# Performance work log

Measured on AMD Instinct MI355X. Metric: run time of the kernel, lower is better.

## Reference

```python
import jax, jax.numpy as jnp
import numpy as np

N = 50000     # nodes
E = 800000    # edges
D = 64        # hidesize (= out_channels per head)
H = 5         # heads
C = 64        # per-head channels (concat=False -> mean over heads, C == D)
NEG_SLOPE = 0.2
LN_EPS = 1e-5


def setup_inputs() -> dict:
    key = jax.random.key(0)
    ks = jax.random.split(key, 16)
    s = 0.05
    return {
        "features": jax.random.normal(ks[0], (N, D), dtype=jnp.float32),
        "edge_index": jax.random.randint(ks[1], (2, E), 0, N, dtype=jnp.int64),
        "rel_emb_vector": jax.random.normal(ks[2], (E, D), dtype=jnp.float32),
        # GATv2Conv params
        "Wl": jax.random.normal(ks[3], (D, H * C), dtype=jnp.float32) * s,
        "bl": jnp.zeros((H * C,), jnp.float32),
        "Wr": jax.random.normal(ks[4], (D, H * C), dtype=jnp.float32) * s,
        "br": jnp.zeros((H * C,), jnp.float32),
        "We": jax.random.normal(ks[5], (D, H * C), dtype=jnp.float32) * s,  # lin_edge, no bias
        "att": jax.random.normal(ks[6], (H, C), dtype=jnp.float32) * s,
        "conv_bias": jnp.zeros((C,), jnp.float32),
        # LayerNorms
        "ln_g": jnp.ones((D,), jnp.float32), "ln_b": jnp.zeros((D,), jnp.float32),
        "ln1_g": jnp.ones((D,), jnp.float32), "ln1_b": jnp.zeros((D,), jnp.float32),
        # MLP (activation resolved to None by the source bug)
        "fc_w": jax.random.normal(ks[7], (D, 2 * D), dtype=jnp.float32) * s,
        "fc_b": jnp.zeros((2 * D,), jnp.float32),
        "fc1_w": jax.random.normal(ks[8], (2 * D, D), dtype=jnp.float32) * s,
        "fc1_b": jnp.zeros((D,), jnp.float32),
    }


def _layernorm(x, g, b):
    m = x.mean(-1, keepdims=True)
    v = ((x - m) ** 2).mean(-1, keepdims=True)
    return (x - m) * jax.lax.rsqrt(v + LN_EPS) * g + b


def _gatv2_conv(x, edge_index, edge_attr, Wl, bl, Wr, br, We, att, conv_bias):
    src, dst = edge_index[0], edge_index[1]
    n = x.shape[0]
    # add_self_loops with fill_value='mean': self-loop edge_attr = mean of incoming edge_attr
    cnt = jax.ops.segment_sum(jnp.ones((edge_attr.shape[0],), x.dtype), dst, num_segments=n)
    loop_attr = jax.ops.segment_sum(edge_attr, dst, num_segments=n) / jnp.maximum(cnt, 1.0)[:, None]
    ar = jnp.arange(n, dtype=src.dtype)
    src2 = jnp.concatenate([src, ar])
    dst2 = jnp.concatenate([dst, ar])
    ea = jnp.concatenate([edge_attr, loop_attr], axis=0)        # [E+N, D]
    xl = (x @ Wl + bl).reshape(n, H, C)                          # source transform
    xr = (x @ Wr + br).reshape(n, H, C)                          # target transform
    em = (ea @ We).reshape(-1, H, C)
    m = jax.nn.leaky_relu(xl[src2] + xr[dst2] + em, NEG_SLOPE)   # [E+N, H, C]
    logits = jnp.einsum('ehc,hc->eh', m, att)                    # [E+N, H]
    # scatter-softmax over destination nodes (self loops guarantee nonempty segments)
    mx = jax.lax.stop_gradient(jax.ops.segment_max(logits, dst2, num_segments=n))
    z = jnp.exp(logits - mx[dst2])
    den = jax.ops.segment_sum(z, dst2, num_segments=n)
    alpha = z / den[dst2]                                        # [E+N, H]
    out = jax.ops.segment_sum(xl[src2] * alpha[:, :, None], dst2, num_segments=n)  # [N, H, C]
    return out.mean(axis=1) + conv_bias                          # concat=False -> head mean


def reference(features, edge_index, rel_emb_vector, Wl, bl, Wr, br, We, att, conv_bias,
              ln_g, ln_b, ln1_g, ln1_b, fc_w, fc_b, fc1_w, fc1_b):
    conv = _gatv2_conv(features, edge_index, rel_emb_vector, Wl, bl, Wr, br, We, att, conv_bias)
    x = _layernorm(features + conv, ln_g, ln_b)
    h = (x @ fc_w + fc_b) @ fc1_w + fc1_b   # activation=None, dropout in eval mode
    return _layernorm(x + h, ln1_g, ln1_b)
```

## Files before the change

kernel.cpp:

```cpp
#include <hip/hip_runtime.h>
#include <hip/hip_bf16.h>
#include <math.h>

#define LN_EPS 1e-5f
#define NEGS 0.2f

typedef short s8v __attribute__((ext_vector_type(8)));
typedef short s4v __attribute__((ext_vector_type(4)));
typedef float f4v __attribute__((ext_vector_type(4)));
typedef unsigned short ushort;

__device__ __forceinline__ float wredsum(float v) {
#pragma unroll
    for (int s = 32; s > 0; s >>= 1) v += __shfl_xor(v, s);
    return v;
}
__device__ __forceinline__ ushort f2bf(float x) {
    union { __hip_bfloat16 h; ushort u; } c;
    c.h = __float2bfloat16(x);
    return c.u;
}
__device__ __forceinline__ float bf2f(ushort u) {
    return __uint_as_float(((unsigned int)u) << 16);
}

__global__ void k_hist(const int* __restrict__ dst, int* __restrict__ cnt, int E) {
    int idx = blockIdx.x * blockDim.x + threadIdx.x;
    int stride = gridDim.x * blockDim.x;
    for (; idx < E; idx += stride) atomicAdd(&cnt[dst[idx]], 1);
}

__global__ __launch_bounds__(1024) void k_scanA(const int* __restrict__ cnt,
                                                int* __restrict__ bsum, int N) {
    __shared__ int ws[16];
    int tt = threadIdx.x, ln = tt & 63, wv = tt >> 6;
    int i = blockIdx.x * 1024 + tt;
    int v = (i < N) ? (cnt[i] + 1) : 0;
#pragma unroll
    for (int s = 32; s > 0; s >>= 1) v += __shfl_xor(v, s);
    if (ln == 0) ws[wv] = v;
    __syncthreads();
    if (tt == 0) {
        int s = 0;
#pragma unroll
        for (int k = 0; k < 16; k++) s += ws[k];
        bsum[blockIdx.x] = s;
    }
}
__global__ __launch_bounds__(64) void k_scanB(const int* __restrict__ bsum,
                                              int* __restrict__ bpre,
                                              int* __restrict__ roffN, int nb) {
    int ln = threadIdx.x;
    int v = (ln < nb) ? bsum[ln] : 0;
    int x = v;
#pragma unroll
    for (int off = 1; off < 64; off <<= 1) {
        int y = __shfl_up(x, off);
        if (ln >= off) x += y;
    }
    if (ln < nb) bpre[ln] = x - v;
    if (ln == 63) *roffN = x;
}
__global__ __launch_bounds__(1024) void k_scanC(const int* __restrict__ cnt,
                                                const int* __restrict__ bpre,
                                                int* __restrict__ roff,
                                                int* __restrict__ wpos, int N) {
    __shared__ int ws[16];
    int tt = threadIdx.x, ln = tt & 63, wv = tt >> 6;
    int i = blockIdx.x * 1024 + tt;
    int v = (i < N) ? (cnt[i] + 1) : 0;
    int x = v;
#pragma unroll
    for (int off = 1; off < 64; off <<= 1) {
        int y = __shfl_up(x, off);
        if (ln >= off) x += y;
    }
    if (ln == 63) ws[wv] = x;
    __syncthreads();
    if (wv == 0) {
        int wsv = (ln < 16) ? ws[ln] : 0;
        int xs = wsv;
#pragma unroll
        for (int off = 1; off < 16; off <<= 1) {
            int y = __shfl_up(xs, off);
            if (ln >= off) xs += y;
        }
        if (ln < 16) ws[ln] = xs - wsv;
    }
    __syncthreads();
    int excl = x - v + ws[wv] + bpre[blockIdx.x];
    if (i < N) { roff[i] = excl; wpos[i] = excl; }
}

__global__ void k_scatter(const int* __restrict__ src, const int* __restrict__ dst,
                          int* __restrict__ wpos, int* __restrict__ eidC,
                          int* __restrict__ srcC, int* __restrict__ posC, int E) {
    int idx = blockIdx.x * blockDim.x + threadIdx.x;
    int stride = gridDim.x * blockDim.x;
    for (; idx < E; idx += stride) {
        int d = dst[idx];
        int p = atomicAdd(&wpos[d], 1);
        eidC[p] = idx;
        srcC[p] = src[idx];
        posC[idx] = p;
    }
}

__global__ __launch_bounds__(256) void k_loopcsr(const int* __restrict__ eidC,
                                                 const int* __restrict__ roff,
                                                 const float* __restrict__ rel,
                                                 float* __restrict__ loopat,
                                                 int* __restrict__ srcC, int N) {
    int t = threadIdx.x, ln = t & 63, wv = t >> 6;
    int nw = gridDim.x * 4;
    for (int n = blockIdx.x * 4 + wv; n < N; n += nw) {
        int r0 = roff[n], r1 = roff[n + 1];
        int deg = r1 - r0 - 1;
        float s0 = 0.f, s1 = 0.f, s2 = 0.f, s3 = 0.f;
        int j = 0;
        for (; j + 4 <= deg; j += 4) {
            int e0 = eidC[r0 + j], e1 = eidC[r0 + j + 1];
            int e2 = eidC[r0 + j + 2], e3 = eidC[r0 + j + 3];
            s0 += rel[(long long)e0 * 64 + ln];
            s1 += rel[(long long)e1 * 64 + ln];
            s2 += rel[(long long)e2 * 64 + ln];
            s3 += rel[(long long)e3 * 64 + ln];
        }
        for (; j < deg; j++) s0 += rel[(long long)eidC[r0 + j] * 64 + ln];
        float s = (s0 + s1) + (s2 + s3);
        loopat[(long long)n * 64 + ln] = s / (float)(deg > 0 ? deg : 1);
        if (ln == 0) srcC[r1 - 1] = n;
    }
}

__global__ __launch_bounds__(512) void k_linC(const float* __restrict__ feat,
                                              const float* __restrict__ Wlg,
                                              const float* __restrict__ blg,
                                              const float* __restrict__ Wrg,
                                              const float* __restrict__ brg,
                                              ushort* __restrict__ xlbf,
                                              ushort* __restrict__ xrbf, int N) {
    __shared__ __align__(16) ushort wT[2][64 * 320];
    int t = threadIdx.x;
    for (int i = t; i < 5120; i += 512) {
        int mat = i >= 2560;
        int j = mat ? (i - 2560) : i;
        int n = j >> 3, kb = j & 7;
        const float* W = mat ? Wrg : Wlg;
        s8v v;
#pragma unroll
        for (int k = 0; k < 8; k++) v[k] = (short)f2bf(W[(kb * 8 + k) * 320 + n]);
        int by = (n * 128 + kb * 16) ^ ((n & 7) << 4);
        *(s8v*)((char*)&wT[mat][0] + by) = v;
    }
    __syncthreads();

    int l = t & 63, wv = t >> 6;
    int g = l >> 4, m = l & 15;
    int wstride = gridDim.x * 128;
    for (int r0 = (blockIdx.x * 8 + wv) * 16; r0 < N; r0 += wstride) {
        s8v afr[2];
        {
            long long row = (r0 + m < N) ? (r0 + m) : (N - 1);
#pragma unroll
            for (int kh = 0; kh < 2; kh++) {
                const float* p = feat + row * 64 + kh * 32 + g * 8;
                float4 u0 = *(const float4*)(p);
                float4 u1 = *(const float4*)(p + 4);
                s8v a;
                a[0] = (short)f2bf(u0.x); a[1] = (short)f2bf(u0.y);
                a[2] = (short)f2bf(u0.z); a[3] = (short)f2bf(u0.w);
                a[4] = (short)f2bf(u1.x); a[5] = (short)f2bf(u1.y);
                a[6] = (short)f2bf(u1.z); a[7] = (short)f2bf(u1.w);
                afr[kh] = a;
            }
        }
#pragma unroll
        for (int mat = 0; mat < 2; mat++) {
            const float* bias = mat ? brg : blg;
            ushort* y = mat ? xrbf : xlbf;
            const char* wb = (const char*)&wT[mat][0];
#pragma unroll
            for (int h = 0; h < 5; h++) {
                f4v acc[4];
#pragma unroll
                for (int ct = 0; ct < 4; ct++) acc[ct] = (f4v)0.0f;
#pragma unroll
                for (int ct = 0; ct < 4; ct++) {
                    int n = h * 64 + ct * 16 + m;
                    int b0 = (n * 128 + 0 * 64 + g * 16) ^ ((n & 7) << 4);
                    int b1 = (n * 128 + 1 * 64 + g * 16) ^ ((n & 7) << 4);
                    s8v bf0 = *(const s8v*)(wb + b0);
                    s8v bf1 = *(const s8v*)(wb + b1);
                    acc[ct] = __builtin_amdgcn_mfma_f32_16x16x32_bf16(afr[0], bf0, acc[ct], 0, 0, 0);
                    acc[ct] = __builtin_amdgcn_mfma_f32_16x16x32_bf16(afr[1], bf1, acc[ct], 0, 0, 0);
                }
                float bv[4];
#pragma unroll
                for (int ct = 0; ct < 4; ct++) bv[ct] = bias[h * 64 + ct * 16 + m];
#pragma unroll
                for (int q = 0; q < 4; q++) {
                    int row = r0 + g * 4 + q;
                    if (row < N) {
                        s4v o;
#pragma unroll
                        for (int ct = 0; ct < 4; ct++) o[ct] = (short)f2bf(acc[ct][q] + bv[ct]);
                        *(s4v*)(y + (long long)row * 320 + h * 64 + m * 4) = o;
                    }
                }
            }
        }
    }
}

__global__ __launch_bounds__(512) void k_fused(
    const float* __restrict__ rel, const float* __restrict__ loopat,
    const int* __restrict__ src, const int* __restrict__ dst,
    const ushort* __restrict__ xlbf, const ushort* __restrict__ xrbf,
    const float* __restrict__ Weg, const float* __restrict__ attg,
    const int* __restrict__ posC, const int* __restrict__ roff,
    float* __restrict__ logitsC, int E, int M) {
    __shared__ __align__(16) ushort weT[64 * 320];
    int t = threadIdx.x;
    for (int i = t; i < 2560; i += 512) {
        int n = i >> 3, kb = i & 7;
        s8v v;
#pragma unroll
        for (int k = 0; k < 8; k++) v[k] = (short)f2bf(Weg[(kb * 8 + k) * 320 + n]);
        int by = (n * 128 + kb * 16) ^ ((n & 7) << 4);
        *(s8v*)((char*)weT + by) = v;
    }
    __syncthreads();

    int l = t & 63, wv = t >> 6;
    int g = l >> 4, m = l & 15;
    int r0 = (blockIdx.x * 8 + wv) * 16;
    if (r0 >= M) return;

    s8v afr[2];
    {
        int row = r0 + m;
        if (row >= M) row = M - 1;
        const float* ap = (row < E) ? (rel + (long long)row * 64)
                                    : (loopat + (long long)(row - E) * 64);
#pragma unroll
        for (int kh = 0; kh < 2; kh++) {
            const float* p = ap + kh * 32 + g * 8;
            float4 u0 = *(const float4*)(p);
            float4 u1 = *(const float4*)(p + 4);
            s8v a;
            a[0] = (short)f2bf(u0.x); a[1] = (short)f2bf(u0.y);
            a[2] = (short)f2bf(u0.z); a[3] = (short)f2bf(u0.w);
            a[4] = (short)f2bf(u1.x); a[5] = (short)f2bf(u1.y);
            a[6] = (short)f2bf(u1.z); a[7] = (short)f2bf(u1.w);
            afr[kh] = a;
        }
    }

    const ushort* xptr[4];
    const ushort* rptr[4];
    int parr[4];
    bool vld[4];
#pragma unroll
    for (int q = 0; q < 4; q++) {
        int row = r0 + g * 4 + q;
        vld[q] = row < M;
        int rr = vld[q] ? row : (M - 1);
        int s, d, p;
        if (rr < E) { s = src[rr]; d = dst[rr]; p = posC[rr]; }
        else        { s = d = rr - E; p = roff[rr - E + 1] - 1; }
        xptr[q] = xlbf + (long long)s * 320 + m * 4;
        rptr[q] = xrbf + (long long)d * 320 + m * 4;
        parr[q] = p;
    }

    s4v xb[2][4], rb[2][4];
    float attb[2][4];
#pragma unroll
    for (int q = 0; q < 4; q++) {
        xb[0][q] = *(const s4v*)(xptr[q]);
        rb[0][q] = *(const s4v*)(rptr[q]);
    }
#pragma unroll
    for (int ct = 0; ct < 4; ct++) attb[0][ct] = attg[ct * 16 + m];

#pragma unroll
    for (int h = 0; h < 5; h++) {
        if (h < 4) {
#pragma unroll
            for (int q = 0; q < 4; q++) {
                xb[(h + 1) & 1][q] = *(const s4v*)(xptr[q] + (h + 1) * 64);
                rb[(h + 1) & 1][q] = *(const s4v*)(rptr[q] + (h + 1) * 64);
            }
#pragma unroll
            for (int ct = 0; ct < 4; ct++)
                attb[(h + 1) & 1][ct] = attg[(h + 1) * 64 + ct * 16 + m];
        }

        f4v acc[4];
#pragma unroll
        for (int ct = 0; ct < 4; ct++) acc[ct] = (f4v)0.0f;
#pragma unroll
        for (int ct = 0; ct < 4; ct++) {
            int n = h * 64 + ct * 16 + m;
            int b0 = (n * 128 + 0 * 64 + g * 16) ^ ((n & 7) << 4);
            int b1 = (n * 128 + 1 * 64 + g * 16) ^ ((n & 7) << 4);
            s8v bf0 = *(const s8v*)((const char*)weT + b0);
            s8v bf1 = *(const s8v*)((const char*)weT + b1);
            acc[ct] = __builtin_amdgcn_mfma_f32_16x16x32_bf16(afr[0], bf0, acc[ct], 0, 0, 0);
            acc[ct] = __builtin_amdgcn_mfma_f32_16x16x32_bf16(afr[1], bf1, acc[ct], 0, 0, 0);
        }

#pragma unroll
        for (int q = 0; q < 4; q++) {
            float sum = 0.f;
#pragma unroll
            for (int ct = 0; ct < 4; ct++) {
                float v = acc[ct][q] + bf2f((ushort)xb[h & 1][q][ct])
                                     + bf2f((ushort)rb[h & 1][q][ct]);
                v = v > 0.f ? v : v * NEGS;
                sum = fmaf(v, attb[h & 1][ct], sum);
            }
            sum += __shfl_xor(sum, 1);
            sum += __shfl_xor(sum, 2);
            sum += __shfl_xor(sum, 4);
            sum += __shfl_xor(sum, 8);
            if (vld[q] && m == 0) logitsC[(long long)parr[q] * 5 + h] = sum;
        }
    }
}

__global__ __launch_bounds__(256) void k_agg(const float* __restrict__ logitsC,
                                             const int* __restrict__ srcC,
                                             const int* __restrict__ roff,
                                             const ushort* __restrict__ xlbf,
                                             float* __restrict__ conv, int N) {
    int t = threadIdx.x, ln = t & 63, wv = t >> 6;
    int sub = ln >> 4, m = ln & 15;
    int nw = gridDim.x * 4;
    for (int n = blockIdx.x * 4 + wv; n < N; n += nw) {
        int r0 = roff[n], r1 = roff[n + 1];
        int deg = r1 - r0;
        float se[5] = {0.f, 0.f, 0.f, 0.f, 0.f};
        for (int j = ln; j < deg; j += 64) {
            long long base = (long long)(r0 + j) * 5;
#pragma unroll
            for (int h = 0; h < 5; h++) se[h] += expf(logitsC[base + h]);
        }
        float dh[5];
#pragma unroll
        for (int h = 0; h < 5; h++) dh[h] = 1.0f / wredsum(se[h]);
        float accv[4] = {0.f, 0.f, 0.f, 0.f};
        for (int jj = sub; jj < deg; jj += 4) {
            int slot = r0 + jj;
            int s = srcC[slot];
            const ushort* xp = xlbf + (long long)s * 320 + m * 4;
            long long lb = (long long)slot * 5;
#pragma unroll
            for (int h = 0; h < 5; h++) {
                float a = expf(logitsC[lb + h]) * dh[h];
                s4v xv = *(const s4v*)(xp + h * 64);
#pragma unroll
                for (int j = 0; j < 4; j++) accv[j] = fmaf(a, bf2f((ushort)xv[j]), accv[j]);
            }
        }
#pragma unroll
        for (int j = 0; j < 4; j++) {
            accv[j] += __shfl_xor(accv[j], 16);
            accv[j] += __shfl_xor(accv[j], 32);
        }
        float v0 = __shfl(accv[0], m);
        float v1 = __shfl(accv[1], m);
        float v2 = __shfl(accv[2], m);
        float v3 = __shfl(accv[3], m);
        float outv = (sub == 0) ? v0 : (sub == 1) ? v1 : (sub == 2) ? v2 : v3;
        conv[(long long)n * 64 + ln] = outv * 0.2f;
    }
}

__global__ __launch_bounds__(512) void k_mlp(const float* __restrict__ feat,
                                             const float* __restrict__ conv,
                                             const float* __restrict__ cbias,
                                             const float* __restrict__ lng,
                                             const float* __restrict__ lnb,
                                             const float* __restrict__ ln1g,
                                             const float* __restrict__ ln1b,
                                             const float* __restrict__ fcwg,
                                             const float* __restrict__ fcb,
                                             const float* __restrict__ fc1wg,
                                             const float* __restrict__ fc1b,
                                             float* __restrict__ out, int N) {
    __shared__ __align__(16) ushort w1T[64 * 128];
    __shared__ __align__(16) ushort w2T[64 * 128];
    __shared__ __align__(16) ushort tls[8][16 * 128];
    __shared__ __align__(16) ushort xnl[8][16 * 64];
    int t = threadIdx.x;
    for (int i = t; i < 8192; i += 512) {
        int k = i >> 7, n = i & 127;
        int by = (n * 128 + k * 2) ^ ((n & 7) << 4);
        w1T[by >> 1] = f2bf(fcwg[i]);
    }
    for (int i = t; i < 8192; i += 512) {
        int k = i >> 6, n = i & 63;
        int by = (n * 256 + k * 2) ^ ((n & 7) << 4);
        w2T[by >> 1] = f2bf(fc1wg[i]);
    }
    __syncthreads();
    int ln = t & 63, wv = t >> 6;
    int g = ln >> 4, m = ln & 15;
    char* tb = (char*)&tls[wv][0];
    char* xb = (char*)&xnl[wv][0];
    float fcbv[8];
#pragma unroll
    for (int ct = 0; ct < 8; ct++) fcbv[ct] = fcb[ct * 16 + m];
    float fc1bv[4], g1v[4], b1v[4];
#pragma unroll
    for (int ct = 0; ct < 4; ct++) {
        fc1bv[ct] = fc1b[ct * 16 + m];
        g1v[ct] = ln1g[ct * 16 + m];
        b1v[ct] = ln1b[ct * 16 + m];
    }
    int nblk = gridDim.x * 8;
    for (int nb0 = (blockIdx.x * 8 + wv) * 16; nb0 < N; nb0 += nblk * 16) {
        int node = nb0 + m;
        long long nd = (node < N) ? node : (N - 1);
        float xv[2][8];
#pragma unroll
        for (int kh = 0; kh < 2; kh++) {
            int c0 = kh * 32 + g * 8;
            const float* fp = feat + nd * 64 + c0;
            const float* cp = conv + nd * 64 + c0;
            float4 f0 = *(const float4*)fp, f1 = *(const float4*)(fp + 4);
            float4 q0 = *(const float4*)cp, q1 = *(const float4*)(cp + 4);
            float4 cb0 = *(const float4*)(cbias + c0), cb1 = *(const float4*)(cbias + c0 + 4);
            xv[kh][0] = f0.x + q0.x + cb0.x; xv[kh][1] = f0.y + q0.y + cb0.y;
            xv[kh][2] = f0.z + q0.z + cb0.z; xv[kh][3] = f0.w + q0.w + cb0.w;
            xv[kh][4] = f1.x + q1.x + cb1.x; xv[kh][5] = f1.y + q1.y + cb1.y;
            xv[kh][6] = f1.z + q1.z + cb1.z; xv[kh][7] = f1.w + q1.w + cb1.w;
        }
        float sm = 0.f;
#pragma unroll
        for (int kh = 0; kh < 2; kh++)
#pragma unroll
            for (int j = 0; j < 8; j++) sm += xv[kh][j];
        sm += __shfl_xor(sm, 16); sm += __shfl_xor(sm, 32);
        float mu = sm * (1.0f / 64.0f);
        float vr = 0.f;
#pragma unroll
        for (int kh = 0; kh < 2; kh++)
#pragma unroll
            for (int j = 0; j < 8; j++) {
                float dv = xv[kh][j] - mu;
                vr += dv * dv;
            }
        vr += __shfl_xor(vr, 16); vr += __shfl_xor(vr, 32);
        float rs = rsqrtf(vr * (1.0f / 64.0f) + LN_EPS);
        s8v af[2];
#pragma unroll
        for (int kh = 0; kh < 2; kh++) {
            int c0 = kh * 32 + g * 8;
            float4 g0 = *(const float4*)(lng + c0), g1 = *(const float4*)(lng + c0 + 4);
            float4 e0 = *(const float4*)(lnb + c0), e1 = *(const float4*)(lnb + c0 + 4);
            float gg[8] = {g0.x, g0.y, g0.z, g0.w, g1.x, g1.y, g1.z, g1.w};
            float bb[8] = {e0.x, e0.y, e0.z, e0.w, e1.x, e1.y, e1.z, e1.w};
#pragma unroll
            for (int j = 0; j < 8; j++)
                af[kh][j] = (short)f2bf((xv[kh][j] - mu) * rs * gg[j] + bb[j]);
            int by = (m * 128 + (kh * 32 + g * 8) * 2) ^ ((m & 7) << 4);
            *(s8v*)(xb + by) = af[kh];
        }
        f4v a1[8];
#pragma unroll
        for (int ct = 0; ct < 8; ct++) a1[ct] = (f4v)0.0f;
#pragma unroll
        for (int ct = 0; ct < 8; ct++) {
            int n1 = ct * 16 + m;
#pragma unroll
            for (int kh = 0; kh < 2; kh++) {
                int by = (n1 * 128 + (kh * 32 + g * 8) * 2) ^ ((n1 & 7) << 4);
                s8v bf = *(const s8v*)((const char*)w1T + by);
                a1[ct] = __builtin_amdgcn_mfma_f32_16x16x32_bf16(af[kh], bf, a1[ct], 0, 0, 0);
            }
        }
#pragma unroll
        for (int ct = 0; ct < 8; ct++)
#pragma unroll
            for (int q = 0; q < 4; q++) {
                int r = g * 4 + q, c = ct * 16 + m;
                int by = (r * 256 + c * 2) ^ ((r & 7) << 4);
                *(ushort*)(tb + by) = f2bf(a1[ct][q] + fcbv[ct]);
            }
        f4v a2[4];
#pragma unroll
        for (int ct = 0; ct < 4; ct++) a2[ct] = (f4v)0.0f;
#pragma unroll
        for (int kh2 = 0; kh2 < 4; kh2++) {
            int by = (m * 256 + (kh2 * 32 + g * 8) * 2) ^ ((m & 7) << 4);
            s8v a2f = *(const s8v*)(tb + by);
#pragma unroll
            for (int ct = 0; ct < 4; ct++) {
                int n2 = ct * 16 + m;
                int by2 = (n2 * 256 + (kh2 * 32 + g * 8) * 2) ^ ((n2 & 7) << 4);
                s8v bf = *(const s8v*)((const char*)w2T + by2);
                a2[ct] = __builtin_amdgcn_mfma_f32_16x16x32_bf16(a2f, bf, a2[ct], 0, 0, 0);
            }
        }
#pragma unroll
        for (int q = 0; q < 4; q++) {
            int r = g * 4 + q;
            float yv[4];
#pragma unroll
            for (int ct = 0; ct < 4; ct++) {
                int by = (r * 128 + (ct * 16 + m) * 2) ^ ((r & 7) << 4);
                yv[ct] = bf2f(*(const ushort*)(xb + by)) + a2[ct][q] + fc1bv[ct];
            }
            float sm2 = (yv[0] + yv[1]) + (yv[2] + yv[3]);
            sm2 += __shfl_xor(sm2, 1); sm2 += __shfl_xor(sm2, 2);
            sm2 += __shfl_xor(sm2, 4); sm2 += __shfl_xor(sm2, 8);
            float mu2 = sm2 * (1.0f / 64.0f);
            float vr2 = 0.f;
#pragma unroll
            for (int ct = 0; ct < 4; ct++) {
                float dv = yv[ct] - mu2;
                vr2 += dv * dv;
            }
            vr2 += __shfl_xor(vr2, 1); vr2 += __shfl_xor(vr2, 2);
            vr2 += __shfl_xor(vr2, 4); vr2 += __shfl_xor(vr2, 8);
            float rs2 = rsqrtf(vr2 * (1.0f / 64.0f) + LN_EPS);
            int rn = nb0 + r;
            if (rn < N) {
#pragma unroll
                for (int ct = 0; ct < 4; ct++)
                    out[(long long)rn * 64 + ct * 16 + m] =
                        (yv[ct] - mu2) * rs2 * g1v[ct] + b1v[ct];
            }
        }
    }
}

extern "C" void kernel_launch(void* const* d_in, const int* in_sizes, int n_in,
                              void* d_out, int out_size, void* d_ws, size_t ws_size,
                              hipStream_t stream) {
    const float* feat = (const float*)d_in[0];
    const int* ei = (const int*)d_in[1];
    const float* rel = (const float*)d_in[2];
    const float* Wl = (const float*)d_in[3];
    const float* bl = (const float*)d_in[4];
    const float* Wr = (const float*)d_in[5];
    const float* br = (const float*)d_in[6];
    const float* We = (const float*)d_in[7];
    const float* att = (const float*)d_in[8];
    const float* cbias = (const float*)d_in[9];
    const float* lng = (const float*)d_in[10];
    const float* lnb = (const float*)d_in[11];
    const float* ln1g = (const float*)d_in[12];
    const float* ln1b = (const float*)d_in[13];
    const float* fcw = (const float*)d_in[14];
    const float* fcb = (const float*)d_in[15];
    const float* fc1w = (const float*)d_in[16];
    const float* fc1b = (const float*)d_in[17];
    float* out = (float*)d_out;

    int N = in_sizes[0] / 64;
    int E = in_sizes[1] / 2;
    int M = E + N;
    const int* src = ei;
    const int* dst = ei + E;
    int nb = (N + 1023) / 1024;

    char* wsb = (char*)d_ws;
    ushort* xlbf = (ushort*)wsb;            wsb += (size_t)N * 320 * 2;
    ushort* xrbf = (ushort*)wsb;            wsb += (size_t)N * 320 * 2;
    float* loopat = (float*)wsb;            wsb += (size_t)N * 64 * 4;
    float* conv = (float*)wsb;              wsb += (size_t)N * 64 * 4;
    float* logitsC = (float*)wsb;           wsb += (size_t)M * 5 * 4;
    int* cnt = (int*)wsb;                   wsb += (size_t)N * 4;
    int* roff = (int*)wsb;                  wsb += (size_t)(N + 1) * 4;
    int* wpos = (int*)wsb;                  wsb += (size_t)N * 4;
    int* eidC = (int*)wsb;                  wsb += (size_t)M * 4;
    int* srcC = (int*)wsb;                  wsb += (size_t)M * 4;
    int* posC = (int*)wsb;                  wsb += (size_t)E * 4;
    int* bsum = (int*)wsb;                  wsb += 64 * 4;
    int* bpre = (int*)wsb;                  wsb += 64 * 4;

    hipMemsetAsync(cnt, 0, (size_t)N * 4, stream);

    k_hist<<<1024, 256, 0, stream>>>(dst, cnt, E);
    k_scanA<<<nb, 1024, 0, stream>>>(cnt, bsum, N);
    k_scanB<<<1, 64, 0, stream>>>(bsum, bpre, &roff[N], nb);
    k_scanC<<<nb, 1024, 0, stream>>>(cnt, bpre, roff, wpos, N);
    k_scatter<<<1024, 256, 0, stream>>>(src, dst, wpos, eidC, srcC, posC, E);
    k_loopcsr<<<2048, 256, 0, stream>>>(eidC, roff, rel, loopat, srcC, N);
    k_linC<<<(N + 127) / 128, 512, 0, stream>>>(feat, Wl, bl, Wr, br, xlbf, xrbf, N);
    k_fused<<<(M + 127) / 128, 512, 0, stream>>>(rel, loopat, src, dst, xlbf, xrbf, We, att,
                                                 posC, roff, logitsC, E, M);
    k_agg<<<2048, 256, 0, stream>>>(logitsC, srcC, roff, xlbf, conv, N);
    k_mlp<<<391, 512, 0, stream>>>(feat, conv, cbias, lng, lnb, ln1g, ln1b, fcw, fcb, fc1w, fc1b,
                                   out, N);
}
```

Baseline: 598.6 us.

## Iterate fused edge kernel in CSR order and use bit-trick bf16 conversion

The fused edge-logit kernel now walks edges in destination-sorted CSR slot order. It reads eidC/srcC/dstC arrays and writes logits contiguously instead of scattering through posC. The scatter kernel stores dstC rather than posC, and the self-loop slot fills eidC/srcC/dstC. This makes the xr gathers and logit writes more local, at the cost of an indirect gather of rel rows through eidC. The float-to-bf16 conversion is also replaced with an inline round-to-nearest-even bit manipulation, which does not handle NaN specially.

```diff
diff --git a/kernel.cpp b/kernel.cpp
--- a/kernel.cpp
+++ b/kernel.cpp
@@ -16,9 +16,9 @@
     return v;
 }
 __device__ __forceinline__ ushort f2bf(float x) {
-    union { __hip_bfloat16 h; ushort u; } c;
-    c.h = __float2bfloat16(x);
-    return c.u;
+    unsigned int u = __float_as_uint(x);
+    u += 0x7fffu + ((u >> 16) & 1u);
+    return (ushort)(u >> 16);
 }
 __device__ __forceinline__ float bf2f(ushort u) {
     return __uint_as_float(((unsigned int)u) << 16);
@@ -94,7 +94,7 @@
 
 __global__ void k_scatter(const int* __restrict__ src, const int* __restrict__ dst,
                           int* __restrict__ wpos, int* __restrict__ eidC,
-                          int* __restrict__ srcC, int* __restrict__ posC, int E) {
+                          int* __restrict__ srcC, int* __restrict__ dstC, int E) {
     int idx = blockIdx.x * blockDim.x + threadIdx.x;
     int stride = gridDim.x * blockDim.x;
     for (; idx < E; idx += stride) {
@@ -102,15 +102,17 @@
         int p = atomicAdd(&wpos[d], 1);
         eidC[p] = idx;
         srcC[p] = src[idx];
-        posC[idx] = p;
-    }
-}
-
-__global__ __launch_bounds__(256) void k_loopcsr(const int* __restrict__ eidC,
+        dstC[p] = d;
+    }
+}
+
+__global__ __launch_bounds__(256) void k_loopcsr(const int* __restrict__ eidC_ro,
                                                  const int* __restrict__ roff,
                                                  const float* __restrict__ rel,
                                                  float* __restrict__ loopat,
-                                                 int* __restrict__ srcC, int N) {
+                                                 int* __restrict__ eidC,
+                                                 int* __restrict__ srcC,
+                                                 int* __restrict__ dstC, int N, int E) {
     int t = threadIdx.x, ln = t & 63, wv = t >> 6;
     int nw = gridDim.x * 4;
     for (int n = blockIdx.x * 4 + wv; n < N; n += nw) {
@@ -119,17 +121,21 @@
         float s0 = 0.f, s1 = 0.f, s2 = 0.f, s3 = 0.f;
         int j = 0;
         for (; j + 4 <= deg; j += 4) {
-            int e0 = eidC[r0 + j], e1 = eidC[r0 + j + 1];
-            int e2 = eidC[r0 + j + 2], e3 = eidC[r0 + j + 3];
+            int e0 = eidC_ro[r0 + j], e1 = eidC_ro[r0 + j + 1];
+            int e2 = eidC_ro[r0 + j + 2], e3 = eidC_ro[r0 + j + 3];
             s0 += rel[(long long)e0 * 64 + ln];
             s1 += rel[(long long)e1 * 64 + ln];
             s2 += rel[(long long)e2 * 64 + ln];
             s3 += rel[(long long)e3 * 64 + ln];
         }
-        for (; j < deg; j++) s0 += rel[(long long)eidC[r0 + j] * 64 + ln];
+        for (; j < deg; j++) s0 += rel[(long long)eidC_ro[r0 + j] * 64 + ln];
         float s = (s0 + s1) + (s2 + s3);
         loopat[(long long)n * 64 + ln] = s / (float)(deg > 0 ? deg : 1);
-        if (ln == 0) srcC[r1 - 1] = n;
+        if (ln == 0) {
+            eidC[r1 - 1] = E + n;
+            srcC[r1 - 1] = n;
+            dstC[r1 - 1] = n;
+        }
     }
 }
 
@@ -215,10 +221,10 @@
 
 __global__ __launch_bounds__(512) void k_fused(
     const float* __restrict__ rel, const float* __restrict__ loopat,
-    const int* __restrict__ src, const int* __restrict__ dst,
+    const int* __restrict__ eidC, const int* __restrict__ srcC,
+    const int* __restrict__ dstC,
     const ushort* __restrict__ xlbf, const ushort* __restrict__ xrbf,
     const float* __restrict__ Weg, const float* __restrict__ attg,
-    const int* __restrict__ posC, const int* __restrict__ roff,
     float* __restrict__ logitsC, int E, int M) {
     __shared__ __align__(16) ushort weT[64 * 320];
     int t = threadIdx.x;
@@ -239,10 +245,11 @@
 
     s8v afr[2];
     {
-        int row = r0 + m;
-        if (row >= M) row = M - 1;
-        const float* ap = (row < E) ? (rel + (long long)row * 64)
-                                    : (loopat + (long long)(row - E) * 64);
+        int slot = r0 + m;
+        if (slot >= M) slot = M - 1;
+        int e = eidC[slot];
+        const float* ap = (e < E) ? (rel + (long long)e * 64)
+                                  : (loopat + (long long)(e - E) * 64);
 #pragma unroll
         for (int kh = 0; kh < 2; kh++) {
             const float* p = ap + kh * 32 + g * 8;
@@ -259,19 +266,17 @@
 
     const ushort* xptr[4];
     const ushort* rptr[4];
-    int parr[4];
     bool vld[4];
+    int sarr[4];
 #pragma unroll
     for (int q = 0; q < 4; q++) {
-        int row = r0 + g * 4 + q;
-        vld[q] = row < M;
-        int rr = vld[q] ? row : (M - 1);
-        int s, d, p;
-        if (rr < E) { s = src[rr]; d = dst[rr]; p = posC[rr]; }
-        else        { s = d = rr - E; p = roff[rr - E + 1] - 1; }
+        int slot = r0 + g * 4 + q;
+        vld[q] = slot < M;
+        int ss = vld[q] ? slot : (M - 1);
+        sarr[q] = ss;
+        int s = srcC[ss], d = dstC[ss];
         xptr[q] = xlbf + (long long)s * 320 + m * 4;
         rptr[q] = xrbf + (long long)d * 320 + m * 4;
-        parr[q] = p;
     }
 
     s4v xb[2][4], rb[2][4];
@@ -325,7 +330,7 @@
             sum += __shfl_xor(sum, 2);
             sum += __shfl_xor(sum, 4);
             sum += __shfl_xor(sum, 8);
-            if (vld[q] && m == 0) logitsC[(long long)parr[q] * 5 + h] = sum;
+            if (vld[q] && m == 0) logitsC[(long long)sarr[q] * 5 + h] = sum;
         }
     }
 }
@@ -579,7 +584,7 @@
     int* wpos = (int*)wsb;                  wsb += (size_t)N * 4;
     int* eidC = (int*)wsb;                  wsb += (size_t)M * 4;
     int* srcC = (int*)wsb;                  wsb += (size_t)M * 4;
-    int* posC = (int*)wsb;                  wsb += (size_t)E * 4;
+    int* dstC = (int*)wsb;                  wsb += (size_t)M * 4;
     int* bsum = (int*)wsb;                  wsb += 64 * 4;
     int* bpre = (int*)wsb;                  wsb += 64 * 4;
 
@@ -589,11 +594,11 @@
     k_scanA<<<nb, 1024, 0, stream>>>(cnt, bsum, N);
     k_scanB<<<1, 64, 0, stream>>>(bsum, bpre, &roff[N], nb);
     k_scanC<<<nb, 1024, 0, stream>>>(cnt, bpre, roff, wpos, N);
-    k_scatter<<<1024, 256, 0, stream>>>(src, dst, wpos, eidC, srcC, posC, E);
-    k_loopcsr<<<2048, 256, 0, stream>>>(eidC, roff, rel, loopat, srcC, N);
+    k_scatter<<<1024, 256, 0, stream>>>(src, dst, wpos, eidC, srcC, dstC, E);
+    k_loopcsr<<<2048, 256, 0, stream>>>(eidC, roff, rel, loopat, eidC, srcC, dstC, N, E);
     k_linC<<<(N + 127) / 128, 512, 0, stream>>>(feat, Wl, bl, Wr, br, xlbf, xrbf, N);
-    k_fused<<<(M + 127) / 128, 512, 0, stream>>>(rel, loopat, src, dst, xlbf, xrbf, We, att,
-                                                 posC, roff, logitsC, E, M);
+    k_fused<<<(M + 127) / 128, 512, 0, stream>>>(rel, loopat, eidC, srcC, dstC,
+                                                 xlbf, xrbf, We, att, logitsC, E, M);
     k_agg<<<2048, 256, 0, stream>>>(logitsC, srcC, roff, xlbf, conv, N);
     k_mlp<<<391, 512, 0, stream>>>(feat, conv, cbias, lng, lnb, ln1g, ln1b, fcw, fcb, fc1w, fc1b,
                                    out, N);
```

After: 605.7 us. No clear change (+1.2%).
